# Kernel tuning notes

Measured on AMD Instinct MI355X. Metric: run time of the kernel, lower is better.

Reference implementation:

```python
import jax, jax.numpy as jnp
import numpy as np

NUDGE = 1e-7

def _norm(x):
    # global mean + L2-norm over axes (1,2), per sample (faithful to source)
    size = x.shape[1] * x.shape[2]
    mean = jnp.sum(x, axis=(1, 2), keepdims=True) / size
    xc = x - mean
    l2 = jnp.sqrt(jnp.sum(xc * xc, axis=(1, 2), keepdims=True))
    return xc / (l2 + NUDGE)


def setup_inputs() -> dict:
    key = jax.random.key(0)
    ks = jax.random.split(key, 9)
    B, D, S, F = 8, 512, 4096, 2048
    s = 0.02
    x = jax.random.normal(ks[0], (B, D, S), dtype=jnp.float32)
    Wq = jax.random.normal(ks[1], (D, D), dtype=jnp.float32) * s
    Wk = jax.random.normal(ks[2], (D, D), dtype=jnp.float32) * s
    Wv = jax.random.normal(ks[3], (D, D), dtype=jnp.float32) * s
    Wo = jax.random.normal(ks[4], (D, D), dtype=jnp.float32) * s
    W1 = jax.random.normal(ks[5], (D, F), dtype=jnp.float32) * s
    b1 = jnp.zeros((F,), dtype=jnp.float32)
    W2 = jax.random.normal(ks[6], (F, D), dtype=jnp.float32) * s
    b2 = jnp.zeros((D,), dtype=jnp.float32)
    return {"x": x, "Wq": Wq, "Wk": Wk, "Wv": Wv, "Wo": Wo,
            "W1": W1, "b1": b1, "W2": W2, "b2": b2}


def reference(x, Wq, Wk, Wv, Wo, W1, b1, W2, b2):
    B, D, S = x.shape
    xt = jnp.swapaxes(x, 1, 2)                      # [B,S,D]
    q = xt @ Wq                                     # [B,S,D]
    k = xt @ Wk
    v = xt @ Wv
    scores = jnp.einsum('bsd,btd->bst', q, k) / jnp.sqrt(jnp.float32(D))
    attn = jax.nn.softmax(scores, axis=-1)          # [B,S,S]
    attn_out = jnp.swapaxes((attn @ v) @ Wo, 1, 2)  # [B,D,S]

    post = _norm(x + attn_out)                      # [B,D,S]

    # per-slice feedforward+linear loop == batched matmul over token axis
    pt = jnp.swapaxes(post, 1, 2)                   # [B,S,D]
    h = jax.nn.relu(pt @ W1 + b1) @ W2 + b2         # [B,S,D]
    return _norm(post + jnp.swapaxes(h, 1, 2))
```

## Files before the change

kernel.cpp:

```cpp
#include <hip/hip_runtime.h>


typedef unsigned short u16;
typedef __attribute__((ext_vector_type(4))) float f32x4;
typedef __attribute__((ext_vector_type(8))) short s16x8;

__device__ __forceinline__ float bf2f(u16 u) {
    unsigned int v = ((unsigned int)u) << 16;
    float f;
    __builtin_memcpy(&f, &v, 4);
    return f;
}
__device__ __forceinline__ u16 f2bf(float f) {
    unsigned int v;
    __builtin_memcpy(&v, &f, 4);
    unsigned int r = (v + 0x7fffu + ((v >> 16) & 1u)) >> 16;
    return (u16)r;
}
__device__ __forceinline__ u16 loadbf(const void* p, long long i, int f32) {
    return f32 ? f2bf(((const float*)p)[i]) : ((const u16*)p)[i];
}

#if defined(__has_builtin)
#if __has_builtin(__builtin_amdgcn_global_load_lds)
#define HAS_GLDS 1
#endif
#endif
#ifndef HAS_GLDS
#define HAS_GLDS 0
#endif

#if HAS_GLDS
__device__ __forceinline__ void glds16(const u16* g, u16* l) {
    __builtin_amdgcn_global_load_lds(
        (const __attribute__((address_space(1))) void*)g,
        (__attribute__((address_space(3))) void*)l, 16, 0, 0);
}
#else
__device__ __forceinline__ void glds16(const u16* g, u16* l) {
    *(int4*)l = *(const int4*)g;
}
#endif

struct DetectArgs { const u16* p[9]; int n[9]; };

__global__ __launch_bounds__(256) void detect9(DetectArgs a, int* __restrict__ flags)
{
    const u16* p = a.p[blockIdx.x];
    const int n_u16 = a.n[blockIdx.x];
    int insane = 0;
    for (int i = threadIdx.x; i < n_u16; i += 256) {
        u16 h = p[i];
        int e = (h >> 7) & 0xFF;
        int m = h & 0x7F;
        bool sane = (e >= 96 && e <= 141) || (e == 0 && m == 0);
        insane += sane ? 0 : 1;
    }
#pragma unroll
    for (int off = 32; off > 0; off >>= 1) insane += __shfl_down(insane, off);
    __shared__ int red[4];
    if ((threadIdx.x & 63) == 0) red[threadIdx.x >> 6] = insane;
    __syncthreads();
    if (threadIdx.x == 0)
        flags[blockIdx.x] = (red[0] + red[1] + red[2] + red[3] > n_u16 / 4) ? 1 : 0;
}

#define BM 128
#define BN 128
#define BK 32

template <typename OutT, bool BIAS, bool RELU>
__global__ __launch_bounds__(256) void gemm_bt(
    const u16* __restrict__ A, const u16* __restrict__ Bt, OutT* __restrict__ C,
    const u16* __restrict__ bias, int M, int N, int K,
    int lda, int ldb, int ldc, int wmod,
    long long aZ, long long aW, long long bZ, long long bW, long long cZ,
    int swz)
{
    __shared__ u16 As[2][BM * BK];
    __shared__ u16 Bs[2][BN * BK];

    const int z = blockIdx.z;
    const int g = z / wmod, w = z - g * wmod;
    A  += g * aZ + w * aW;
    Bt += g * bZ + w * bW;
    C  += (long long)z * cZ;

    int bx = blockIdx.x, by = blockIdx.y;
    if (swz) {
        const int gx = gridDim.x;
        int id = by * gx + bx;
        int xcd = id & 7, j = id >> 3;
        bx = j % gx;
        by = (j / gx) * 8 + xcd;
    }

    const int tid = threadIdx.x;
    const int wave = tid >> 6, lane = tid & 63;
    const int wm = wave >> 1, wn = wave & 1;
    const int q = lane >> 4, r = lane & 15;

    const int ar = tid >> 2;
    const int ac = (((tid & 3) ^ ((tid >> 3) & 3)) << 3);
    const int ks = (r >> 1) & 3;

    const u16* Ag = A + (long long)(by * BM + ar) * lda + ac;
    const u16* Bg = Bt + (long long)(bx * BN + ar) * ldb + ac;
    const long long rstepA = 64LL * lda, rstepB = 64LL * ldb;

    f32x4 acc[4][4];
    const f32x4 zero = {0.f, 0.f, 0.f, 0.f};
#pragma unroll
    for (int i = 0; i < 4; ++i)
#pragma unroll
        for (int j = 0; j < 4; ++j) acc[i][j] = zero;

    const int nIter = K / BK;
    glds16(Ag, &As[0][tid * 8]);
    glds16(Ag + rstepA, &As[0][2048 + tid * 8]);
    glds16(Bg, &Bs[0][tid * 8]);
    glds16(Bg + rstepB, &Bs[0][2048 + tid * 8]);
    Ag += BK; Bg += BK;
    __syncthreads();
    for (int it = 0; it < nIter; ++it) {
        const int cur = it & 1, nxt = cur ^ 1;
        if (it + 1 < nIter) {
            glds16(Ag, &As[nxt][tid * 8]);
            glds16(Ag + rstepA, &As[nxt][2048 + tid * 8]);
            glds16(Bg, &Bs[nxt][tid * 8]);
            glds16(Bg + rstepB, &Bs[nxt][2048 + tid * 8]);
            Ag += BK; Bg += BK;
        }
        s16x8 af[4], bf[4];
#pragma unroll
        for (int mi = 0; mi < 4; ++mi)
            af[mi] = *(const s16x8*)(&As[cur][(wm * 64 + mi * 16 + r) * BK + ((q ^ ks) << 3)]);
#pragma unroll
        for (int ni = 0; ni < 4; ++ni)
            bf[ni] = *(const s16x8*)(&Bs[cur][(wn * 64 + ni * 16 + r) * BK + ((q ^ ks) << 3)]);
#pragma unroll
        for (int mi = 0; mi < 4; ++mi)
#pragma unroll
            for (int ni = 0; ni < 4; ++ni)
                acc[mi][ni] = __builtin_amdgcn_mfma_f32_16x16x32_bf16(
                    af[mi], bf[ni], acc[mi][ni], 0, 0, 0);
        __syncthreads();
    }

    const int col0 = bx * BN + wn * 64;
    const int row0 = by * BM + wm * 64;
#pragma unroll
    for (int ni = 0; ni < 4; ++ni) {
        const int colg = col0 + ni * 16 + r;
        float bv = 0.f;
        if constexpr (BIAS) bv = bf2f(bias[colg]);
#pragma unroll
        for (int mi = 0; mi < 4; ++mi) {
#pragma unroll
            for (int rr = 0; rr < 4; ++rr) {
                const int rowg = row0 + mi * 16 + q * 4 + rr;
                float v = acc[mi][ni][rr] + bv;
                if constexpr (RELU) v = fmaxf(v, 0.f);
                if constexpr (sizeof(OutT) == 2)
                    C[(long long)rowg * ldc + colg] = (OutT)f2bf(v);
                else
                    C[(long long)rowg * ldc + colg] = (OutT)v;
            }
        }
    }
}

template <bool DIRECT>
__global__ __launch_bounds__(512, 2) void flash_attn(
    const u16* __restrict__ QKV,
    const u16* __restrict__ Vt,
    u16* __restrict__ O,
    float* __restrict__ Opart,
    float* __restrict__ rsPart,
    int nsplit)
{
    __shared__ u16 Qs[64 * 512];
    __shared__ u16 Ks[2][128 * 128];
    __shared__ u16 Ps[64 * 136];
    __shared__ float rsL[8][64];

    const long long SD = 4096LL * 512;
    const int g = blockIdx.z, sp = blockIdx.y;
    const int q0 = blockIdx.x * 64;
    const u16* Qg = QKV + ((long long)g * 3 + 0) * SD;
    const u16* Kg = QKV + ((long long)g * 3 + 1) * SD;
    const u16* Vg = Vt + (long long)g * SD;

    const int tid = threadIdx.x;
    const int wave = tid >> 6, lane = tid & 63;
    const int q = lane >> 4, r = lane & 15;
    const int mg = wave >> 2, ng = wave & 3;
    const int dg = wave;

#pragma unroll
    for (int i = 0; i < 8; ++i) {
        int L = i * 512 + tid;
        int row = L >> 6, p = L & 63;
        int l = p ^ (row & 15);
        glds16(Qg + (long long)(q0 + row) * 512 + l * 8, &Qs[L * 8]);
    }

    f32x4 oacc[4][4];
    const f32x4 zero = {0.f, 0.f, 0.f, 0.f};
#pragma unroll
    for (int i = 0; i < 4; ++i)
#pragma unroll
        for (int j = 0; j < 4; ++j) oacc[i][j] = zero;
    float rsum[2][4] = {{0.f, 0.f, 0.f, 0.f}, {0.f, 0.f, 0.f, 0.f}};

    const int span = 4096 / nsplit;
    const int kt0 = sp * span;
    const int ktN = span / 128;
    const float scale = 0.044194173824159216f;

    auto stageK = [&](int ktile, int kc, int buf) {
#pragma unroll
        for (int i = 0; i < 4; ++i) {
            int L = i * 512 + tid;
            int row = L >> 4, p = L & 15;
            int l = p ^ (row & 15);
            glds16(Kg + (long long)(kt0 + ktile * 128 + row) * 512 + kc * 128 + l * 8,
                   &Ks[buf][L * 8]);
        }
    };
    stageK(0, 0, 0);

    for (int kt = 0; kt < ktN; ++kt) {
        f32x4 sacc[2][2];
#pragma unroll
        for (int i = 0; i < 2; ++i)
#pragma unroll
            for (int j = 0; j < 2; ++j) sacc[i][j] = zero;

        for (int kc = 0; kc < 4; ++kc) {
            if (kc < 3) stageK(kt, kc + 1, (kc + 1) & 1);
            __syncthreads();
            const u16* Kb = Ks[kc & 1];
#pragma unroll
            for (int sc = 0; sc < 4; ++sc) {
                s16x8 af[2], bf[2];
#pragma unroll
                for (int mi = 0; mi < 2; ++mi) {
                    int row = (mg * 2 + mi) * 16 + r;
                    int l = kc * 16 + sc * 4 + q;
                    af[mi] = *(const s16x8*)&Qs[row * 512 + ((l ^ r) << 3)];
                }
#pragma unroll
                for (int ni = 0; ni < 2; ++ni) {
                    int row = (ng * 2 + ni) * 16 + r;
                    int l = sc * 4 + q;
                    bf[ni] = *(const s16x8*)&Kb[row * 128 + ((l ^ r) << 3)];
                }
#pragma unroll
                for (int mi = 0; mi < 2; ++mi)
#pragma unroll
                    for (int ni = 0; ni < 2; ++ni)
                        sacc[mi][ni] = __builtin_amdgcn_mfma_f32_16x16x32_bf16(
                            af[mi], bf[ni], sacc[mi][ni], 0, 0, 0);
            }
        }
#pragma unroll
        for (int mi = 0; mi < 2; ++mi) {
#pragma unroll
            for (int ni = 0; ni < 2; ++ni) {
                int col = (ng * 2 + ni) * 16 + r;
#pragma unroll
                for (int rr = 0; rr < 4; ++rr) {
                    int row = (mg * 2 + mi) * 16 + q * 4 + rr;
                    float v = __expf(fminf(sacc[mi][ni][rr] * scale, 30.f));
                    Ps[row * 136 + col] = f2bf(v);
                    rsum[mi][rr] += v;
                }
            }
        }
        if (kt + 1 < ktN) stageK(kt + 1, 0, 0);
        __syncthreads();
        const long long vbase = (long long)(dg * 64 + r) * 4096 + kt0 + kt * 128;
#pragma unroll
        for (int kc = 0; kc < 4; ++kc) {
            s16x8 af[4], bf[4];
#pragma unroll
            for (int mi = 0; mi < 4; ++mi)
                af[mi] = *(const s16x8*)(Vg + vbase + (long long)mi * 16 * 4096
                                         + kc * 32 + q * 8);
#pragma unroll
            for (int ni = 0; ni < 4; ++ni)
                bf[ni] = *(const s16x8*)&Ps[(ni * 16 + r) * 136 + kc * 32 + q * 8];
#pragma unroll
            for (int mi = 0; mi < 4; ++mi)
#pragma unroll
                for (int ni = 0; ni < 4; ++ni)
                    oacc[mi][ni] = __builtin_amdgcn_mfma_f32_16x16x32_bf16(
                        af[mi], bf[ni], oacc[mi][ni], 0, 0, 0);
        }
    }

#pragma unroll
    for (int mi = 0; mi < 2; ++mi)
#pragma unroll
        for (int rr = 0; rr < 4; ++rr) {
            float s = rsum[mi][rr];
#pragma unroll
            for (int m = 1; m < 16; m <<= 1) s += __shfl_xor(s, m);
            rsum[mi][rr] = s;
        }
    if (r == 0) {
#pragma unroll
        for (int mi = 0; mi < 2; ++mi)
#pragma unroll
            for (int rr = 0; rr < 4; ++rr)
                rsL[wave][(mg * 2 + mi) * 16 + q * 4 + rr] = rsum[mi][rr];
    }
    __syncthreads();

    if constexpr (DIRECT) {
        u16* Og = O + (long long)g * SD;
#pragma unroll
        for (int ni = 0; ni < 4; ++ni) {
            int qrow = ni * 16 + r;
            int wb = (qrow >> 5) * 4;
            float rs = rsL[wb][qrow] + rsL[wb + 1][qrow]
                     + rsL[wb + 2][qrow] + rsL[wb + 3][qrow];
            float inv = 1.f / rs;
#pragma unroll
            for (int mi = 0; mi < 4; ++mi) {
                int d = (dg * 4 + mi) * 16 + q * 4;
                ushort4 o4;
                o4.x = f2bf(oacc[mi][ni][0] * inv);
                o4.y = f2bf(oacc[mi][ni][1] * inv);
                o4.z = f2bf(oacc[mi][ni][2] * inv);
                o4.w = f2bf(oacc[mi][ni][3] * inv);
                *(ushort4*)&Og[(long long)(q0 + qrow) * 512 + d] = o4;
            }
        }
    } else {
        const int pb = g * nsplit + sp;
        float* Op = Opart + (long long)pb * SD;
#pragma unroll
        for (int ni = 0; ni < 4; ++ni) {
            int qrow = ni * 16 + r;
#pragma unroll
            for (int mi = 0; mi < 4; ++mi) {
                int d = (dg * 4 + mi) * 16 + q * 4;
                float4 o4;
                o4.x = oacc[mi][ni][0]; o4.y = oacc[mi][ni][1];
                o4.z = oacc[mi][ni][2]; o4.w = oacc[mi][ni][3];
                *(float4*)&Op[(long long)(q0 + qrow) * 512 + d] = o4;
            }
        }
        if (tid < 64) {
            int wb = (tid >> 5) * 4;
            rsPart[(long long)pb * 4096 + q0 + tid] =
                rsL[wb][tid] + rsL[wb + 1][tid] + rsL[wb + 2][tid] + rsL[wb + 3][tid];
        }
    }
}

__global__ __launch_bounds__(256) void reduce_flash(
    const float* __restrict__ Opart, const float* __restrict__ rsPart,
    u16* __restrict__ O, int ns)
{
    const long long SD = 4096LL * 512;
    const int g = blockIdx.y;
    u16* Og = O + (long long)g * SD;
    const int base = blockIdx.x * 2048;
#pragma unroll
    for (int it = 0; it < 8; ++it) {
        int i = base + it * 256 + threadIdx.x;
        int row = i >> 9;
        float s = 0.f, rs = 0.f;
        for (int sp = 0; sp < ns; ++sp) {
            s += Opart[(long long)(g * ns + sp) * SD + i];
            rs += rsPart[(long long)(g * ns + sp) * 4096 + row];
        }
        Og[i] = f2bf(s / rs);
    }
}

__global__ __launch_bounds__(256) void transpose_any(
    const void* __restrict__ in, u16* __restrict__ out, int R, int C,
    long long sIn, long long sOut, const int* __restrict__ flag)
{
    __shared__ u16 tile[32][33];
    const int f32 = *flag;
    const long long ib = (long long)blockIdx.z * sIn;
    u16* ob = out + (long long)blockIdx.z * sOut;
    const int c0 = blockIdx.x * 32, r0 = blockIdx.y * 32;
    const int tx = threadIdx.x, ty = threadIdx.y;
#pragma unroll
    for (int i = 0; i < 4; ++i) {
        int rr = ty + i * 8;
        tile[rr][tx] = loadbf(in, ib + (long long)(r0 + rr) * C + c0 + tx, f32);
    }
    __syncthreads();
#pragma unroll
    for (int i = 0; i < 4; ++i) {
        int cc = ty + i * 8;
        ob[(long long)(c0 + cc) * R + r0 + tx] = tile[tx][cc];
    }
}

__global__ __launch_bounds__(256) void transpose_b16(
    const u16* __restrict__ in, u16* __restrict__ out, int R, int C,
    long long sIn, long long sOut)
{
    __shared__ u16 tile[32][33];
    in += (long long)blockIdx.z * sIn;
    out += (long long)blockIdx.z * sOut;
    const int c0 = blockIdx.x * 32, r0 = blockIdx.y * 32;
    const int tx = threadIdx.x, ty = threadIdx.y;
#pragma unroll
    for (int i = 0; i < 4; ++i) {
        int rr = ty + i * 8;
        tile[rr][tx] = in[(long long)(r0 + rr) * C + c0 + tx];
    }
    __syncthreads();
#pragma unroll
    for (int i = 0; i < 4; ++i) {
        int cc = ty + i * 8;
        out[(long long)(c0 + cc) * R + r0 + tx] = tile[tx][cc];
    }
}

__global__ __launch_bounds__(256) void convert_bias(
    const void* __restrict__ b1, const void* __restrict__ b2,
    u16* __restrict__ ob, const int* __restrict__ f1, const int* __restrict__ f2)
{
    int i = blockIdx.x * 256 + threadIdx.x;
    if (i < 2048) ob[i] = loadbf(b1, i, *f1);
    else if (i < 2560) ob[i] = loadbf(b2, i - 2048, *f2);
}

__global__ __launch_bounds__(256) void stats_add_partial(
    const u16* __restrict__ A, const u16* __restrict__ Bv,
    float2* __restrict__ partial)
{
    const int b = blockIdx.y;
    const long long yb = (long long)b * (4096LL * 512);
    const int base = blockIdx.x * 2048;
    float s = 0.f, ss = 0.f;
#pragma unroll
    for (int it = 0; it < 8; ++it) {
        int i = base + it * 256 + threadIdx.x;
        float z = bf2f(A[yb + i]) + bf2f(Bv[yb + i]);
        s += z; ss += z * z;
    }
#pragma unroll
    for (int off = 32; off > 0; off >>= 1) {
        s += __shfl_down(s, off); ss += __shfl_down(ss, off);
    }
    __shared__ float red[8];
    int lane = threadIdx.x & 63, wave = threadIdx.x >> 6;
    if (lane == 0) { red[wave * 2] = s; red[wave * 2 + 1] = ss; }
    __syncthreads();
    if (threadIdx.x == 0) {
        for (int w = 1; w < 4; ++w) { s += red[w * 2]; ss += red[w * 2 + 1]; }
        partial[b * 1024 + blockIdx.x] = make_float2(s, ss);
    }
}

__global__ __launch_bounds__(256) void stats_finish(
    const float2* __restrict__ partial, float2* __restrict__ stats, float N)
{
    const int b = blockIdx.x;
    float s = 0.f, ss = 0.f;
    for (int i = threadIdx.x; i < 1024; i += 256) {
        float2 p = partial[b * 1024 + i];
        s += p.x; ss += p.y;
    }
#pragma unroll
    for (int off = 32; off > 0; off >>= 1) {
        s += __shfl_down(s, off); ss += __shfl_down(ss, off);
    }
    __shared__ float red[8];
    int lane = threadIdx.x & 63, wave = threadIdx.x >> 6;
    if (lane == 0) { red[wave * 2] = s; red[wave * 2 + 1] = ss; }
    __syncthreads();
    if (threadIdx.x == 0) {
        for (int w = 1; w < 4; ++w) { s += red[w * 2]; ss += red[w * 2 + 1]; }
        float mean = s / N;
        float l2 = sqrtf(fmaxf(ss - s * s / N, 0.f));
        stats[b] = make_float2(mean, 1.f / (l2 + 1e-7f));
    }
}

__global__ __launch_bounds__(256) void post_kernel(
    const u16* __restrict__ A, const u16* __restrict__ Bv,
    const float2* __restrict__ stats, u16* __restrict__ post)
{
    const int b = blockIdx.y;
    const float2 st = stats[b];
    const long long yb = (long long)b * (4096LL * 512);
    const int base = blockIdx.x * 2048;
#pragma unroll
    for (int it = 0; it < 8; ++it) {
        int i = base + it * 256 + threadIdx.x;
        float z = bf2f(A[yb + i]) + bf2f(Bv[yb + i]);
        post[yb + i] = f2bf((z - st.x) * st.y);
    }
}

__global__ __launch_bounds__(256) void final_kernel(
    const u16* __restrict__ P, const u16* __restrict__ G,
    const float2* __restrict__ stats, float* __restrict__ out)
{
    __shared__ float tile[32][33];
    const int b = blockIdx.z;
    const float2 st = stats[b];
    const long long bb = (long long)b * (4096LL * 512);
    const int s0 = blockIdx.x * 32, d0 = blockIdx.y * 32;
    const int tx = threadIdx.x, ty = threadIdx.y;
#pragma unroll
    for (int i = 0; i < 4; ++i) {
        int sl = ty + i * 8;
        long long idx = bb + (long long)(s0 + sl) * 512 + d0 + tx;
        tile[sl][tx] = bf2f(P[idx]) + bf2f(G[idx]);
    }
    __syncthreads();
#pragma unroll
    for (int i = 0; i < 4; ++i) {
        int dl = ty + i * 8;
        out[bb + (long long)(d0 + dl) * 4096 + s0 + tx] =
            (tile[tx][dl] - st.x) * st.y;
    }
}

extern "C" void kernel_launch(void* const* d_in, const int* in_sizes, int n_in,
                              void* d_out, int out_size, void* d_ws, size_t ws_size,
                              hipStream_t stream)
{
    (void)out_size;
    const void* x  = d_in[0];
    const void* Wq = d_in[1];
    const void* Wk = d_in[2];
    const void* Wv = d_in[3];
    const void* Wo = d_in[4];
    const void* W1 = d_in[5];
    const void* b1 = d_in[6];
    const void* W2 = d_in[7];
    const void* b2 = d_in[8];

    const int Bb = 8, D = 512, S = 4096, F = 2048;
    const long long SD = (long long)S * D;
    const long long DD = (long long)D * D;

    char* ws = (char*)d_ws;
    size_t off = 0;
    auto take = [&](size_t bytes) -> char* {
        char* p = ws + off;
        off += (bytes + 255) & ~(size_t)255;
        return p;
    };
    u16* xt   = (u16*)take((size_t)Bb * SD * 2);
    u16* WqT  = (u16*)take((size_t)DD * 2);
    u16* WkT  = (u16*)take((size_t)DD * 2);
    u16* WvT  = (u16*)take((size_t)DD * 2);
    u16* WoT  = (u16*)take((size_t)DD * 2);
    u16* W1T  = (u16*)take((size_t)D * F * 2);
    u16* W2T  = (u16*)take((size_t)D * F * 2);
    u16* bb   = (u16*)take(2560 * 2);
    u16* post = (u16*)take((size_t)Bb * SD * 2);
    float2* npart  = (float2*)take(8 * 1024 * sizeof(float2));
    float2* stats1v = (float2*)take(256);
    float2* stats2v = (float2*)take(256);
    int* flags = (int*)take(16 * sizeof(int));
    float* rsPart = (float*)take(4 * 4096 * sizeof(float));

    size_t remaining = ws_size > off ? ws_size - off : 0;
    const size_t perG = (size_t)4 * SD * 2 + 4096;
    int G = (remaining >= 8 * perG) ? 8 : (remaining >= 4 * perG) ? 4 : 2;
    int ns = (G >= 4) ? 1 : 2;

    u16* attnBuf = (u16*)take((size_t)4 * G * SD * 2);
    u16* QKVb = attnBuf;
    u16* Vtb  = attnBuf + (size_t)3 * G * SD;
    float* Opart = (float*)post;
    u16* Oall = (u16*)d_out;
    u16* Y    = post;
    u16* Hbuf = (u16*)d_out;
    u16* Gbuf = attnBuf;

    DetectArgs da;
    for (int i = 0; i < 9; ++i) {
        da.p[i] = (const u16*)d_in[i];
        da.n[i] = (i < n_in && in_sizes[i] < 8192) ? in_sizes[i] : 8192;
    }
    detect9<<<dim3(9), 256, 0, stream>>>(da, flags);

    dim3 tb(32, 8, 1);
    transpose_any<<<dim3(S / 32, D / 32, Bb), tb, 0, stream>>>(x, xt, D, S, SD, SD, flags + 0);
    transpose_any<<<dim3(16, 16, 1), tb, 0, stream>>>(Wq, WqT, D, D, 0, 0, flags + 1);
    transpose_any<<<dim3(16, 16, 1), tb, 0, stream>>>(Wk, WkT, D, D, 0, 0, flags + 2);
    transpose_any<<<dim3(16, 16, 1), tb, 0, stream>>>(Wv, WvT, D, D, 0, 0, flags + 3);
    transpose_any<<<dim3(16, 16, 1), tb, 0, stream>>>(Wo, WoT, D, D, 0, 0, flags + 4);
    transpose_any<<<dim3(F / 32, D / 32, 1), tb, 0, stream>>>(W1, W1T, D, F, 0, 0, flags + 5);
    transpose_any<<<dim3(D / 32, F / 32, 1), tb, 0, stream>>>(W2, W2T, F, D, 0, 0, flags + 7);
    convert_bias<<<10, 256, 0, stream>>>(b1, b2, bb, flags + 6, flags + 8);

    for (int b0 = 0; b0 < Bb; b0 += G) {
        gemm_bt<u16, false, false><<<dim3(D / 128, S / 128, 3 * G), 256, 0, stream>>>(
            xt + (long long)b0 * SD, WqT, QKVb, nullptr, S, D, D, D, D, D,
            3, SD, 0, 0, DD, SD, 1);
        transpose_b16<<<dim3(D / 32, S / 32, G), tb, 0, stream>>>(
            QKVb + 2 * SD, Vtb, S, D, 3 * SD, SD);
        if (ns == 1) {
            flash_attn<true><<<dim3(64, 1, G), 512, 0, stream>>>(
                QKVb, Vtb, Oall + (long long)b0 * SD, nullptr, nullptr, 1);
        } else {
            flash_attn<false><<<dim3(64, ns, G), 512, 0, stream>>>(
                QKVb, Vtb, nullptr, Opart, rsPart, ns);
            reduce_flash<<<dim3(1024, G), 256, 0, stream>>>(
                Opart, rsPart, Oall + (long long)b0 * SD, ns);
        }
    }

    gemm_bt<u16, false, false><<<dim3(D / 128, (Bb * S) / 128, 1), 256, 0, stream>>>(
        Oall, WoT, Y, nullptr, Bb * S, D, D, D, D, D, 1, 0, 0, 0, 0, 0, 1);

    stats_add_partial<<<dim3(1024, Bb), 256, 0, stream>>>(xt, Y, npart);
    stats_finish<<<dim3(Bb), 256, 0, stream>>>(npart, stats1v, (float)SD);
    post_kernel<<<dim3(1024, Bb), 256, 0, stream>>>(xt, Y, stats1v, post);

    for (int h = 0; h < 2; ++h) {
        gemm_bt<u16, true, true><<<dim3(F / 128, (4 * S) / 128, 1), 256, 0, stream>>>(
            post + (long long)h * 4 * SD, W1T, Hbuf, bb, 4 * S, F, D, D, D, F,
            1, 0, 0, 0, 0, 0, 1);
        gemm_bt<u16, true, false><<<dim3(D / 128, (4 * S) / 128, 1), 256, 0, stream>>>(
            Hbuf, W2T, Gbuf + (long long)h * 4 * SD, bb + 2048, 4 * S, D, F, F, F, D,
            1, 0, 0, 0, 0, 0, 1);
    }

    stats_add_partial<<<dim3(1024, Bb), 256, 0, stream>>>(post, Gbuf, npart);
    stats_finish<<<dim3(Bb), 256, 0, stream>>>(npart, stats2v, (float)SD);
    final_kernel<<<dim3(S / 32, D / 32, Bb), tb, 0, stream>>>(
        post, Gbuf, stats2v, (float*)d_out);
}
```

Measured before the change: 1.022 ms.

## Shrink flash-attention tiles to 32 queries by 64 keys for higher occupancy

Halves the query tile to 32 rows and the key tile to 64, which cuts LDS use and accumulator registers so four 512-thread blocks can target each CU instead of two, and doubles the grid. It also remaps block indices so consecutive blocks interleave batch groups, moves a barrier so the K buffer is not overwritten while still being read, and raises wave priority around the PV MFMA loop. The cost is that each K/V tile is reused across fewer queries, so global and L2 traffic for K and V roughly doubles, and each loop iteration has more barriers relative to compute.

```diff
diff --git a/kernel.cpp b/kernel.cpp
--- a/kernel.cpp
+++ b/kernel.cpp
@@ -171,7 +171,7 @@
 }
 
 template <bool DIRECT>
-__global__ __launch_bounds__(512, 2) void flash_attn(
+__global__ __launch_bounds__(512, 4) void flash_attn(
     const u16* __restrict__ QKV,
     const u16* __restrict__ Vt,
     u16* __restrict__ O,
@@ -179,14 +179,19 @@
     float* __restrict__ rsPart,
     int nsplit)
 {
-    __shared__ u16 Qs[64 * 512];
-    __shared__ u16 Ks[2][128 * 128];
-    __shared__ u16 Ps[64 * 136];
-    __shared__ float rsL[8][64];
+    __shared__ u16 Qs[32 * 512];
+    __shared__ u16 Ks[2][64 * 128];
+    __shared__ u16 Ps[32 * 72];
+    __shared__ float rsL[8][32];
 
     const long long SD = 4096LL * 512;
-    const int g = blockIdx.z, sp = blockIdx.y;
-    const int q0 = blockIdx.x * 64;
+    int g = blockIdx.z, qb = blockIdx.x;
+    if (gridDim.z == 8 && gridDim.y == 1) {
+        int id = g * 128 + qb;
+        g = id & 7; qb = id >> 3;
+    }
+    const int sp = blockIdx.y;
+    const int q0 = qb * 32;
     const u16* Qg = QKV + ((long long)g * 3 + 0) * SD;
     const u16* Kg = QKV + ((long long)g * 3 + 1) * SD;
     const u16* Vg = Vt + (long long)g * SD;
@@ -198,138 +203,113 @@
     const int dg = wave;
 
 #pragma unroll
-    for (int i = 0; i < 8; ++i) {
+    for (int i = 0; i < 4; ++i) {
         int L = i * 512 + tid;
         int row = L >> 6, p = L & 63;
         int l = p ^ (row & 15);
         glds16(Qg + (long long)(q0 + row) * 512 + l * 8, &Qs[L * 8]);
     }
 
-    f32x4 oacc[4][4];
+    f32x4 oacc[4][2];
     const f32x4 zero = {0.f, 0.f, 0.f, 0.f};
 #pragma unroll
-    for (int i = 0; i < 4; ++i)
-#pragma unroll
-        for (int j = 0; j < 4; ++j) oacc[i][j] = zero;
-    float rsum[2][4] = {{0.f, 0.f, 0.f, 0.f}, {0.f, 0.f, 0.f, 0.f}};
+    for (int i = 0; i < 4; ++i) { oacc[i][0] = zero; oacc[i][1] = zero; }
+    float rsum[4] = {0.f, 0.f, 0.f, 0.f};
 
     const int span = 4096 / nsplit;
     const int kt0 = sp * span;
-    const int ktN = span / 128;
+    const int ktN = span / 64;
     const float scale = 0.044194173824159216f;
 
     auto stageK = [&](int ktile, int kc, int buf) {
 #pragma unroll
-        for (int i = 0; i < 4; ++i) {
+        for (int i = 0; i < 2; ++i) {
             int L = i * 512 + tid;
             int row = L >> 4, p = L & 15;
             int l = p ^ (row & 15);
-            glds16(Kg + (long long)(kt0 + ktile * 128 + row) * 512 + kc * 128 + l * 8,
+            glds16(Kg + (long long)(kt0 + ktile * 64 + row) * 512 + kc * 128 + l * 8,
                    &Ks[buf][L * 8]);
         }
     };
     stageK(0, 0, 0);
 
     for (int kt = 0; kt < ktN; ++kt) {
-        f32x4 sacc[2][2];
-#pragma unroll
-        for (int i = 0; i < 2; ++i)
-#pragma unroll
-            for (int j = 0; j < 2; ++j) sacc[i][j] = zero;
-
+        f32x4 sacc = zero;
         for (int kc = 0; kc < 4; ++kc) {
+            __syncthreads();
             if (kc < 3) stageK(kt, kc + 1, (kc + 1) & 1);
-            __syncthreads();
             const u16* Kb = Ks[kc & 1];
+            const int qrow = mg * 16 + r;
+            const int krow = ng * 16 + r;
 #pragma unroll
             for (int sc = 0; sc < 4; ++sc) {
-                s16x8 af[2], bf[2];
-#pragma unroll
-                for (int mi = 0; mi < 2; ++mi) {
-                    int row = (mg * 2 + mi) * 16 + r;
-                    int l = kc * 16 + sc * 4 + q;
-                    af[mi] = *(const s16x8*)&Qs[row * 512 + ((l ^ r) << 3)];
-                }
-#pragma unroll
-                for (int ni = 0; ni < 2; ++ni) {
-                    int row = (ng * 2 + ni) * 16 + r;
-                    int l = sc * 4 + q;
-                    bf[ni] = *(const s16x8*)&Kb[row * 128 + ((l ^ r) << 3)];
-                }
-#pragma unroll
-                for (int mi = 0; mi < 2; ++mi)
-#pragma unroll
-                    for (int ni = 0; ni < 2; ++ni)
-                        sacc[mi][ni] = __builtin_amdgcn_mfma_f32_16x16x32_bf16(
-                            af[mi], bf[ni], sacc[mi][ni], 0, 0, 0);
+                int lq = kc * 16 + sc * 4 + q;
+                s16x8 af = *(const s16x8*)&Qs[qrow * 512 + ((lq ^ r) << 3)];
+                int lk = sc * 4 + q;
+                s16x8 bf = *(const s16x8*)&Kb[krow * 128 + ((lk ^ r) << 3)];
+                sacc = __builtin_amdgcn_mfma_f32_16x16x32_bf16(af, bf, sacc, 0, 0, 0);
             }
         }
-#pragma unroll
-        for (int mi = 0; mi < 2; ++mi) {
-#pragma unroll
-            for (int ni = 0; ni < 2; ++ni) {
-                int col = (ng * 2 + ni) * 16 + r;
-#pragma unroll
-                for (int rr = 0; rr < 4; ++rr) {
-                    int row = (mg * 2 + mi) * 16 + q * 4 + rr;
-                    float v = __expf(fminf(sacc[mi][ni][rr] * scale, 30.f));
-                    Ps[row * 136 + col] = f2bf(v);
-                    rsum[mi][rr] += v;
-                }
+        {
+            int col = ng * 16 + r;
+#pragma unroll
+            for (int rr = 0; rr < 4; ++rr) {
+                int row = mg * 16 + q * 4 + rr;
+                float v = __expf(fminf(sacc[rr] * scale, 30.f));
+                Ps[row * 72 + col] = f2bf(v);
+                rsum[rr] += v;
             }
         }
+        __syncthreads();
         if (kt + 1 < ktN) stageK(kt + 1, 0, 0);
-        __syncthreads();
-        const long long vbase = (long long)(dg * 64 + r) * 4096 + kt0 + kt * 128;
-#pragma unroll
-        for (int kc = 0; kc < 4; ++kc) {
-            s16x8 af[4], bf[4];
+        const long long vbase = (long long)(dg * 64 + r) * 4096 + kt0 + kt * 64;
+#pragma unroll
+        for (int kc = 0; kc < 2; ++kc) {
+            s16x8 af[4], bf[2];
 #pragma unroll
             for (int mi = 0; mi < 4; ++mi)
                 af[mi] = *(const s16x8*)(Vg + vbase + (long long)mi * 16 * 4096
                                          + kc * 32 + q * 8);
 #pragma unroll
-            for (int ni = 0; ni < 4; ++ni)
-                bf[ni] = *(const s16x8*)&Ps[(ni * 16 + r) * 136 + kc * 32 + q * 8];
+            for (int ni = 0; ni < 2; ++ni)
+                bf[ni] = *(const s16x8*)&Ps[(ni * 16 + r) * 72 + kc * 32 + q * 8];
+            __builtin_amdgcn_s_setprio(1);
 #pragma unroll
             for (int mi = 0; mi < 4; ++mi)
 #pragma unroll
-                for (int ni = 0; ni < 4; ++ni)
+                for (int ni = 0; ni < 2; ++ni)
                     oacc[mi][ni] = __builtin_amdgcn_mfma_f32_16x16x32_bf16(
                         af[mi], bf[ni], oacc[mi][ni], 0, 0, 0);
-        }
-    }
-
-#pragma unroll
-    for (int mi = 0; mi < 2; ++mi)
-#pragma unroll
-        for (int rr = 0; rr < 4; ++rr) {
-            float s = rsum[mi][rr];
-#pragma unroll
-            for (int m = 1; m < 16; m <<= 1) s += __shfl_xor(s, m);
-            rsum[mi][rr] = s;
-        }
+            __builtin_amdgcn_s_setprio(0);
+        }
+    }
+
+#pragma unroll
+    for (int rr = 0; rr < 4; ++rr) {
+        float s = rsum[rr];
+#pragma unroll
+        for (int m = 1; m < 16; m <<= 1) s += __shfl_xor(s, m);
+        rsum[rr] = s;
+    }
     if (r == 0) {
 #pragma unroll
-        for (int mi = 0; mi < 2; ++mi)
-#pragma unroll
-            for (int rr = 0; rr < 4; ++rr)
-                rsL[wave][(mg * 2 + mi) * 16 + q * 4 + rr] = rsum[mi][rr];
+        for (int rr = 0; rr < 4; ++rr)
+            rsL[wave][mg * 16 + q * 4 + rr] = rsum[rr];
     }
     __syncthreads();
 
     if constexpr (DIRECT) {
         u16* Og = O + (long long)g * SD;
 #pragma unroll
-        for (int ni = 0; ni < 4; ++ni) {
+        for (int ni = 0; ni < 2; ++ni) {
             int qrow = ni * 16 + r;
-            int wb = (qrow >> 5) * 4;
+            int wb = (qrow >> 4) * 4;
             float rs = rsL[wb][qrow] + rsL[wb + 1][qrow]
                      + rsL[wb + 2][qrow] + rsL[wb + 3][qrow];
             float inv = 1.f / rs;
 #pragma unroll
             for (int mi = 0; mi < 4; ++mi) {
-                int d = (dg * 4 + mi) * 16 + q * 4;
+                int d = dg * 64 + mi * 16 + q * 4;
                 ushort4 o4;
                 o4.x = f2bf(oacc[mi][ni][0] * inv);
                 o4.y = f2bf(oacc[mi][ni][1] * inv);
@@ -342,19 +322,19 @@
         const int pb = g * nsplit + sp;
         float* Op = Opart + (long long)pb * SD;
 #pragma unroll
-        for (int ni = 0; ni < 4; ++ni) {
+        for (int ni = 0; ni < 2; ++ni) {
             int qrow = ni * 16 + r;
 #pragma unroll
             for (int mi = 0; mi < 4; ++mi) {
-                int d = (dg * 4 + mi) * 16 + q * 4;
+                int d = dg * 64 + mi * 16 + q * 4;
                 float4 o4;
                 o4.x = oacc[mi][ni][0]; o4.y = oacc[mi][ni][1];
                 o4.z = oacc[mi][ni][2]; o4.w = oacc[mi][ni][3];
                 *(float4*)&Op[(long long)(q0 + qrow) * 512 + d] = o4;
             }
         }
-        if (tid < 64) {
-            int wb = (tid >> 5) * 4;
+        if (tid < 32) {
+            int wb = (tid >> 4) * 4;
             rsPart[(long long)pb * 4096 + q0 + tid] =
                 rsL[wb][tid] + rsL[wb + 1][tid] + rsL[wb + 2][tid] + rsL[wb + 3][tid];
         }
@@ -609,10 +589,10 @@
         transpose_b16<<<dim3(D / 32, S / 32, G), tb, 0, stream>>>(
             QKVb + 2 * SD, Vtb, S, D, 3 * SD, SD);
         if (ns == 1) {
-            flash_attn<true><<<dim3(64, 1, G), 512, 0, stream>>>(
+            flash_attn<true><<<dim3(128, 1, G), 512, 0, stream>>>(
                 QKVb, Vtb, Oall + (long long)b0 * SD, nullptr, nullptr, 1);
         } else {
-            flash_attn<false><<<dim3(64, ns, G), 512, 0, stream>>>(
+            flash_attn<false><<<dim3(128, ns, G), 512, 0, stream>>>(
                 QKVb, Vtb, nullptr, Opart, rsPart, ns);
             reduce_flash<<<dim3(1024, G), 256, 0, stream>>>(
                 Opart, rsPart, Oall + (long long)b0 * SD, ns);
```

Measured after the change: 1.242 ms. 21.5% more time.

## Shrink flash-attention key tile, load K directly from global, raise occupancy

Applied to the files above, without the earlier changes.

The flash attention kernel drops the double-buffered K staging in LDS and reads K fragments straight from global memory, with the key tile shrunk from 128 to 64 and the P buffer shrunk to match. The smaller LDS footprint lets the launch bound request 4 blocks per CU instead of 2. It also remaps block ids so consecutive blocks hit different batches when the grid is unsplit, and raises wave priority around the PV MFMA loop. In exchange, K is now read from global/L2 once per wave with no LDS reuse, and there are extra barriers per tile.

```diff
diff --git a/kernel.cpp b/kernel.cpp
--- a/kernel.cpp
+++ b/kernel.cpp
@@ -171,7 +171,7 @@
 }
 
 template <bool DIRECT>
-__global__ __launch_bounds__(512, 2) void flash_attn(
+__global__ __launch_bounds__(512, 4) void flash_attn(
     const u16* __restrict__ QKV,
     const u16* __restrict__ Vt,
     u16* __restrict__ O,
@@ -180,13 +180,17 @@
     int nsplit)
 {
     __shared__ u16 Qs[64 * 512];
-    __shared__ u16 Ks[2][128 * 128];
-    __shared__ u16 Ps[64 * 136];
+    __shared__ u16 Ps[64 * 72];
     __shared__ float rsL[8][64];
 
     const long long SD = 4096LL * 512;
-    const int g = blockIdx.z, sp = blockIdx.y;
-    const int q0 = blockIdx.x * 64;
+    int g = blockIdx.z, qb = blockIdx.x;
+    if (gridDim.z == 8 && gridDim.y == 1) {
+        int id = g * 64 + qb;
+        g = id & 7; qb = id >> 3;
+    }
+    const int sp = blockIdx.y;
+    const int q0 = qb * 64;
     const u16* Qg = QKV + ((long long)g * 3 + 0) * SD;
     const u16* Kg = QKV + ((long long)g * 3 + 1) * SD;
     const u16* Vg = Vt + (long long)g * SD;
@@ -204,6 +208,7 @@
         int l = p ^ (row & 15);
         glds16(Qg + (long long)(q0 + row) * 512 + l * 8, &Qs[L * 8]);
     }
+    __syncthreads();
 
     f32x4 oacc[4][4];
     const f32x4 zero = {0.f, 0.f, 0.f, 0.f};
@@ -215,88 +220,59 @@
 
     const int span = 4096 / nsplit;
     const int kt0 = sp * span;
-    const int ktN = span / 128;
+    const int ktN = span / 64;
     const float scale = 0.044194173824159216f;
 
-    auto stageK = [&](int ktile, int kc, int buf) {
-#pragma unroll
-        for (int i = 0; i < 4; ++i) {
-            int L = i * 512 + tid;
-            int row = L >> 4, p = L & 15;
-            int l = p ^ (row & 15);
-            glds16(Kg + (long long)(kt0 + ktile * 128 + row) * 512 + kc * 128 + l * 8,
-                   &Ks[buf][L * 8]);
-        }
-    };
-    stageK(0, 0, 0);
-
     for (int kt = 0; kt < ktN; ++kt) {
-        f32x4 sacc[2][2];
-#pragma unroll
-        for (int i = 0; i < 2; ++i)
-#pragma unroll
-            for (int j = 0; j < 2; ++j) sacc[i][j] = zero;
-
-        for (int kc = 0; kc < 4; ++kc) {
-            if (kc < 3) stageK(kt, kc + 1, (kc + 1) & 1);
-            __syncthreads();
-            const u16* Kb = Ks[kc & 1];
-#pragma unroll
-            for (int sc = 0; sc < 4; ++sc) {
-                s16x8 af[2], bf[2];
-#pragma unroll
-                for (int mi = 0; mi < 2; ++mi) {
-                    int row = (mg * 2 + mi) * 16 + r;
-                    int l = kc * 16 + sc * 4 + q;
-                    af[mi] = *(const s16x8*)&Qs[row * 512 + ((l ^ r) << 3)];
-                }
-#pragma unroll
-                for (int ni = 0; ni < 2; ++ni) {
-                    int row = (ng * 2 + ni) * 16 + r;
-                    int l = sc * 4 + q;
-                    bf[ni] = *(const s16x8*)&Kb[row * 128 + ((l ^ r) << 3)];
-                }
-#pragma unroll
-                for (int mi = 0; mi < 2; ++mi)
-#pragma unroll
-                    for (int ni = 0; ni < 2; ++ni)
-                        sacc[mi][ni] = __builtin_amdgcn_mfma_f32_16x16x32_bf16(
-                            af[mi], bf[ni], sacc[mi][ni], 0, 0, 0);
+        f32x4 sacc[2];
+        sacc[0] = zero; sacc[1] = zero;
+        const u16* Kt = Kg + (long long)(kt0 + kt * 64 + ng * 16 + r) * 512;
+#pragma unroll
+        for (int st = 0; st < 16; ++st) {
+            s16x8 bf = *(const s16x8*)(Kt + st * 32 + q * 8);
+#pragma unroll
+            for (int mi = 0; mi < 2; ++mi) {
+                int row = mg * 32 + mi * 16 + r;
+                int l = st * 4 + q;
+                s16x8 af = *(const s16x8*)&Qs[row * 512 + ((l ^ r) << 3)];
+                sacc[mi] = __builtin_amdgcn_mfma_f32_16x16x32_bf16(
+                    af, bf, sacc[mi], 0, 0, 0);
             }
         }
-#pragma unroll
-        for (int mi = 0; mi < 2; ++mi) {
-#pragma unroll
-            for (int ni = 0; ni < 2; ++ni) {
-                int col = (ng * 2 + ni) * 16 + r;
+        __syncthreads();
+        {
+            int col = ng * 16 + r;
+#pragma unroll
+            for (int mi = 0; mi < 2; ++mi) {
 #pragma unroll
                 for (int rr = 0; rr < 4; ++rr) {
-                    int row = (mg * 2 + mi) * 16 + q * 4 + rr;
-                    float v = __expf(fminf(sacc[mi][ni][rr] * scale, 30.f));
-                    Ps[row * 136 + col] = f2bf(v);
+                    int row = mg * 32 + mi * 16 + q * 4 + rr;
+                    float v = __expf(fminf(sacc[mi][rr] * scale, 30.f));
+                    Ps[row * 72 + col] = f2bf(v);
                     rsum[mi][rr] += v;
                 }
             }
         }
-        if (kt + 1 < ktN) stageK(kt + 1, 0, 0);
         __syncthreads();
-        const long long vbase = (long long)(dg * 64 + r) * 4096 + kt0 + kt * 128;
-#pragma unroll
-        for (int kc = 0; kc < 4; ++kc) {
-            s16x8 af[4], bf[4];
+        const long long vbase = (long long)(dg * 64 + r) * 4096 + kt0 + kt * 64;
+#pragma unroll
+        for (int kc = 0; kc < 2; ++kc) {
+            s16x8 af[4], bfp[4];
 #pragma unroll
             for (int mi = 0; mi < 4; ++mi)
                 af[mi] = *(const s16x8*)(Vg + vbase + (long long)mi * 16 * 4096
                                          + kc * 32 + q * 8);
 #pragma unroll
             for (int ni = 0; ni < 4; ++ni)
-                bf[ni] = *(const s16x8*)&Ps[(ni * 16 + r) * 136 + kc * 32 + q * 8];
+                bfp[ni] = *(const s16x8*)&Ps[(ni * 16 + r) * 72 + kc * 32 + q * 8];
+            __builtin_amdgcn_s_setprio(1);
 #pragma unroll
             for (int mi = 0; mi < 4; ++mi)
 #pragma unroll
                 for (int ni = 0; ni < 4; ++ni)
                     oacc[mi][ni] = __builtin_amdgcn_mfma_f32_16x16x32_bf16(
-                        af[mi], bf[ni], oacc[mi][ni], 0, 0, 0);
+                        af[mi], bfp[ni], oacc[mi][ni], 0, 0, 0);
+            __builtin_amdgcn_s_setprio(0);
         }
     }
 
@@ -314,7 +290,7 @@
         for (int mi = 0; mi < 2; ++mi)
 #pragma unroll
             for (int rr = 0; rr < 4; ++rr)
-                rsL[wave][(mg * 2 + mi) * 16 + q * 4 + rr] = rsum[mi][rr];
+                rsL[wave][mg * 32 + mi * 16 + q * 4 + rr] = rsum[mi][rr];
     }
     __syncthreads();
 
@@ -329,7 +305,7 @@
             float inv = 1.f / rs;
 #pragma unroll
             for (int mi = 0; mi < 4; ++mi) {
-                int d = (dg * 4 + mi) * 16 + q * 4;
+                int d = dg * 64 + mi * 16 + q * 4;
                 ushort4 o4;
                 o4.x = f2bf(oacc[mi][ni][0] * inv);
                 o4.y = f2bf(oacc[mi][ni][1] * inv);
@@ -346,7 +322,7 @@
             int qrow = ni * 16 + r;
 #pragma unroll
             for (int mi = 0; mi < 4; ++mi) {
-                int d = (dg * 4 + mi) * 16 + q * 4;
+                int d = dg * 64 + mi * 16 + q * 4;
                 float4 o4;
                 o4.x = oacc[mi][ni][0]; o4.y = oacc[mi][ni][1];
                 o4.z = oacc[mi][ni][2]; o4.w = oacc[mi][ni][3];
```

Result: slower. 1.276 ms (+24.8%).
